# Kernel optimization log

Measured on AMD Instinct MI355X. Metric: run time of the kernel, lower is better.

Reference implementation:

```python
import jax, jax.numpy as jnp
import numpy as np

DIM = 1024
INTER = 1408
N_EXPERTS = 16
TOPK = 2
N_SHARED = 2
SHARED_INTER = N_SHARED * INTER
ROUTE_SCALE = 1.0


def setup_inputs() -> dict:
    key = jax.random.key(0)
    ks = jax.random.split(key, 16)
    s = 0.02
    return {
        "x": jax.random.normal(ks[0], (2, 2048, DIM), dtype=jnp.float32),
        "gate_w": jax.random.normal(ks[1], (DIM, N_EXPERTS), dtype=jnp.float32) * s,
        "gate_b": jnp.zeros((N_EXPERTS,), dtype=jnp.float32),
        "w1": jax.random.normal(ks[2], (N_EXPERTS, DIM, INTER), dtype=jnp.float32) * s,
        "b1": jnp.zeros((N_EXPERTS, INTER), dtype=jnp.float32),
        "w3": jax.random.normal(ks[3], (N_EXPERTS, DIM, INTER), dtype=jnp.float32) * s,
        "b3": jnp.zeros((N_EXPERTS, INTER), dtype=jnp.float32),
        "w2": jax.random.normal(ks[4], (N_EXPERTS, INTER, DIM), dtype=jnp.float32) * s,
        "b2": jnp.zeros((N_EXPERTS, DIM), dtype=jnp.float32),
        "sw1": jax.random.normal(ks[5], (DIM, SHARED_INTER), dtype=jnp.float32) * s,
        "sb1": jax.random.normal(ks[6], (SHARED_INTER,), dtype=jnp.float32) * s,
        "sw3": jax.random.normal(ks[7], (DIM, SHARED_INTER), dtype=jnp.float32) * s,
        "sb3": jax.random.normal(ks[8], (SHARED_INTER,), dtype=jnp.float32) * s,
        "sw2": jax.random.normal(ks[9], (SHARED_INTER, DIM), dtype=jnp.float32) * s,
        "sb2": jax.random.normal(ks[10], (DIM,), dtype=jnp.float32) * s,
    }


def reference(x, gate_w, gate_b, w1, b1, w3, b3, w2, b2, sw1, sb1, sw3, sb3, sw2, sb2):
    shape = x.shape
    xf = x.reshape(-1, DIM)  # [T, D]

    # Gate: softmax scores in fp32, top-k routing
    logits = xf @ gate_w + gate_b  # [T, E]
    scores = jax.nn.softmax(logits.astype(jnp.float32), axis=-1)
    top_vals, top_idx = jax.lax.top_k(scores, TOPK)  # [T, K]
    weights = (top_vals * ROUTE_SCALE).astype(x.dtype)

    # Combine weights per expert: [T, E]; zero for unselected experts
    cw = (jax.nn.one_hot(top_idx, N_EXPERTS, dtype=x.dtype) * weights[..., None]).sum(axis=1)

    # Routed experts (dense-per-expert SwiGLU, masked by combine weights)
    h = jnp.einsum('td,edh->teh', xf, w1) + b1  # [T, E, I]
    g = jnp.einsum('td,edh->teh', xf, w3) + b3
    a = jax.nn.silu(h) * g
    y = jnp.einsum('teh,ehd,te->td', a, w2, cw) + cw @ b2  # [T, D]

    # Shared expert SwiGLU
    z = (jax.nn.silu(xf @ sw1 + sb1) * (xf @ sw3 + sb3)) @ sw2 + sb2

    return (y + z).reshape(shape)
```

## Files before the change

### kernel.cpp

```cpp
#include <hip/hip_runtime.h>
#include <cstdint>
#include <cstddef>

#define T_TOKENS 4096
#define DIM      1024
#define INTER    1408
#define NEXP     16
#define SINTER   2816

typedef uint32_t u32;
typedef uint16_t u16;

using s8v = __attribute__((ext_vector_type(8))) short;
using f4v = __attribute__((ext_vector_type(4))) float;

__device__ __forceinline__ u16 f2bf(float f) {
  u32 u = __float_as_uint(f);
  return (u16)((u + 0x7fffu + ((u >> 16) & 1u)) >> 16);
}
__device__ __forceinline__ u32 pack2(float a, float b) {
  return (u32)f2bf(a) | ((u32)f2bf(b) << 16);
}

__device__ __forceinline__ void load_lds16(const u16* g, u16* l) {
  __builtin_amdgcn_global_load_lds((const __attribute__((address_space(1))) void*)g,
                                   (__attribute__((address_space(3))) void*)l,
                                   16, 0, 0);
}

__global__ __launch_bounds__(256)
void cvt_x(const float* __restrict__ in, u16* __restrict__ out) {
  const int i = (blockIdx.x * 256 + threadIdx.x) * 8;
  float4 a = *(const float4*)(in + i);
  float4 b = *(const float4*)(in + i + 4);
  uint4 o;
  o.x = pack2(a.x, a.y); o.y = pack2(a.z, a.w);
  o.z = pack2(b.x, b.y); o.w = pack2(b.z, b.w);
  *(uint4*)(out + i) = o;
}

__global__ __launch_bounds__(256)
void transpose_cvt(const float* __restrict__ in, u16* __restrict__ out,
                   int K, int N) {
  const size_t eoff = (size_t)blockIdx.z * K * N;
  const int n0 = blockIdx.x * 64, k0 = blockIdx.y * 64;
  __shared__ u16 t[64][72];

  const int tid = threadIdx.x;
  {
    const int r = tid >> 4, c4 = (tid & 15) * 4;
    const float* src = in + eoff + (size_t)k0 * N + n0;
#pragma unroll
    for (int i = 0; i < 4; i++) {
      int row = r + i * 16;
      float4 v = *(const float4*)(src + (size_t)row * N + c4);
      t[c4 + 0][row] = f2bf(v.x);
      t[c4 + 1][row] = f2bf(v.y);
      t[c4 + 2][row] = f2bf(v.z);
      t[c4 + 3][row] = f2bf(v.w);
    }
  }
  __syncthreads();
  {
    const int r = tid >> 3, cc = (tid & 7) * 8;
    u16* dst = out + eoff + (size_t)n0 * K + k0;
#pragma unroll
    for (int i = 0; i < 2; i++) {
      int row = r + i * 32;
      uint4 v = *(const uint4*)&t[row][cc];
      *(uint4*)(dst + (size_t)row * K + cc) = v;
    }
  }
}

__global__ __launch_bounds__(256)
void gate_logits(const float* __restrict__ x, const float* __restrict__ gw,
                 const float* __restrict__ gb,
                 int* __restrict__ g_e, float* __restrict__ g_w)
{
  const int tok  = blockIdx.x * 4 + (threadIdx.x >> 6);
  const int lane = threadIdx.x & 63;
  const int e = lane & 15, s = lane >> 4;
  const float* xr = x + (size_t)tok * DIM;

  float acc = 0.f;
#pragma unroll 8
  for (int i = 0; i < DIM / 4; i++) {
    const int k = i * 4 + s;
    acc = fmaf(xr[k], gw[i * 64 + lane], acc);
  }
  acc += __shfl_xor(acc, 16, 64);
  acc += __shfl_xor(acc, 32, 64);
  const float logit = acc + gb[e];

  float mx = logit;
#pragma unroll
  for (int o = 1; o < 16; o <<= 1) mx = fmaxf(mx, __shfl_xor(mx, o, 64));
  float p = __expf(logit - mx);
  float sum = p;
#pragma unroll
  for (int o = 1; o < 16; o <<= 1) sum += __shfl_xor(sum, o, 64);
  p /= sum;

  float m0 = p; int i0 = e;
#pragma unroll
  for (int o = 1; o < 16; o <<= 1) {
    float om = __shfl_xor(m0, o, 64); int oi = __shfl_xor(i0, o, 64);
    if (om > m0 || (om == m0 && oi < i0)) { m0 = om; i0 = oi; }
  }
  float p1 = (e == i0) ? -1.f : p;
  float m1 = p1; int i1 = e;
#pragma unroll
  for (int o = 1; o < 16; o <<= 1) {
    float om = __shfl_xor(m1, o, 64); int oi = __shfl_xor(i1, o, 64);
    if (om > m1 || (om == m1 && oi < i1)) { m1 = om; i1 = oi; }
  }
  if (lane == 0) {
    g_e[tok * 2 + 0] = i0;  g_e[tok * 2 + 1] = i1;
    g_w[tok * 2 + 0] = m0;  g_w[tok * 2 + 1] = m1;
  }
}

__global__ __launch_bounds__(256)
void route_build(const int* __restrict__ g_e,
                 int* __restrict__ offsets,
                 int* __restrict__ tok_slot, int* __restrict__ slot_of)
{
  __shared__ int hist[256][NEXP + 1];
  __shared__ int base[NEXP + 1];
  const int tid = threadIdx.x;
  const int TPT = T_TOKENS / 256;
  const int t0 = tid * TPT;

#pragma unroll
  for (int e = 0; e < NEXP; e++) hist[tid][e] = 0;
  for (int t = t0; t < t0 + TPT; t++) {
    hist[tid][g_e[t * 2 + 0]]++;
    hist[tid][g_e[t * 2 + 1]]++;
  }
  __syncthreads();
  if (tid < NEXP) {
    int run = 0;
    for (int i = 0; i < 256; i++) { int v = hist[i][tid]; hist[i][tid] = run; run += v; }
    base[tid] = run;
  }
  __syncthreads();
  if (tid == 0) {
    int run = 0;
#pragma unroll
    for (int e = 0; e < NEXP; e++) { int c = base[e]; base[e] = run; offsets[e] = run; run += c; }
    base[NEXP] = run; offsets[NEXP] = run;
  }
  __syncthreads();
  for (int t = t0; t < t0 + TPT; t++) {
#pragma unroll
    for (int k = 0; k < 2; k++) {
      const int e = g_e[t * 2 + k];
      const int slot = base[e] + hist[tid][e]++;
      tok_slot[slot] = t;
      slot_of[t * 2 + k] = slot;
    }
  }
}

template<bool GATHER>
__global__ __launch_bounds__(256, 2)
void ffn_up2(const u16* __restrict__ xbf,
             const u16* __restrict__ w1t, const float* __restrict__ b1p,
             const u16* __restrict__ w3t, const float* __restrict__ b3p,
             int N,
             const int* __restrict__ offsets, const int* __restrict__ tok_slot,
             u16* __restrict__ act)
{
  int e = 0, n0, mt;
  {
    const int lin = blockIdx.x;
    const int per = gridDim.x >> 3;
    const int xcd = lin & 7, pos = lin >> 3;
    if constexpr (GATHER) {
      const int half = per >> 1;
      const int sub = (pos >= half) ? 1 : 0;
      e = xcd * 2 + sub;
      const int idx = pos - sub * half;
      n0 = (idx >> 5) * 128;
      mt = idx & 31;
    } else {
      const int g = xcd * per + pos;
      n0 = (g >> 5) * 128;
      mt = g & 31;
    }
  }
  int rowbase = 0, count = T_TOKENS;
  if constexpr (GATHER) { rowbase = offsets[e]; count = offsets[e + 1] - rowbase; }
  const int m0 = mt * 128;
  if (m0 >= count) return;

  const u16* W1 = w1t + (size_t)e * N * DIM;
  const u16* W3 = w3t + (size_t)e * N * DIM;
  const float* B1 = b1p + (size_t)e * N;
  const float* B3 = b3p + (size_t)e * N;

  __shared__ u16 sA[2][128 * 32];
  __shared__ u16 sB1[2][128 * 32];
  __shared__ u16 sB3[2][128 * 32];

  const int tid = threadIdx.x;
  const int lane = tid & 63;
  const int w = tid >> 6;

  const int kc8 = (lane & 3) * 8;
  const u16* aptr[2]; const u16* b1ptr[2]; const u16* b3ptr[2];
  int ldoff[2];
#pragma unroll
  for (int i = 0; i < 2; i++) {
    const int row = i * 64 + w * 16 + (lane >> 2);
    ldoff[i] = i * 2048 + w * 512 + lane * 8;
    int arow = m0 + row; if (arow > count - 1) arow = count - 1;
    const int tok = GATHER ? tok_slot[rowbase + arow] : arow;
    aptr[i]  = xbf + (size_t)tok * DIM + kc8;
    const int brow = n0 + row;
    b1ptr[i] = W1 + (size_t)brow * DIM + kc8;
    b3ptr[i] = W3 + (size_t)brow * DIM + kc8;
  }

  const int ln = lane & 15, q = lane >> 4;
  const int wm = (w & 1) * 64, wn = (w >> 1) * 64;
  const int paOff = (wm + ln) * 32 + q * 8;
  const int pbOff = (wn + ln) * 32 + q * 8;

  f4v acc1[4][4] = {};
  f4v acc3[4][4] = {};

  auto stage = [&](int buf, int k0) {
#pragma unroll
    for (int i = 0; i < 2; i++) {
      load_lds16(aptr[i]  + k0, &sA[buf][ldoff[i]]);
      load_lds16(b1ptr[i] + k0, &sB1[buf][ldoff[i]]);
      load_lds16(b3ptr[i] + k0, &sB3[buf][ldoff[i]]);
    }
  };

  stage(0, 0);
  __syncthreads();
  int cur = 0;
  for (int k0 = 32; k0 <= DIM; k0 += 32) {
    if (k0 < DIM) stage(cur ^ 1, k0);

    const u16* pa  = sA[cur]  + paOff;
    const u16* pb1 = sB1[cur] + pbOff;
    const u16* pb3 = sB3[cur] + pbOff;
    s8v af[4];
#pragma unroll
    for (int i = 0; i < 4; i++) af[i] = *(const s8v*)(pa + i * 512);
#pragma unroll
    for (int j = 0; j < 4; j++) {
      s8v bf1 = *(const s8v*)(pb1 + j * 512);
#pragma unroll
      for (int i = 0; i < 4; i++)
        acc1[i][j] = __builtin_amdgcn_mfma_f32_16x16x32_bf16(af[i], bf1, acc1[i][j], 0, 0, 0);
      s8v bf3 = *(const s8v*)(pb3 + j * 512);
#pragma unroll
      for (int i = 0; i < 4; i++)
        acc3[i][j] = __builtin_amdgcn_mfma_f32_16x16x32_bf16(af[i], bf3, acc3[i][j], 0, 0, 0);
    }
    __syncthreads();
    cur ^= 1;
  }

  float bb1[4], bb3[4];
#pragma unroll
  for (int j = 0; j < 4; j++) {
    const int col = n0 + wn + j * 16 + ln;
    bb1[j] = B1[col]; bb3[j] = B3[col];
  }
#pragma unroll
  for (int i = 0; i < 4; i++) {
#pragma unroll
    for (int r = 0; r < 4; r++) {
      const int row = m0 + wm + i * 16 + q * 4 + r;
      if (row >= count) continue;
      u16* ap = act + (size_t)(rowbase + row) * N + n0 + wn;
#pragma unroll
      for (int j = 0; j < 4; j++) {
        float h = acc1[i][j][r] + bb1[j];
        float g = acc3[i][j][r] + bb3[j];
        float sv = 1.f / (1.f + __expf(-h));
        ap[j * 16 + ln] = f2bf(h * sv * g);
      }
    }
  }
}

template<bool ROUTED>
__global__ __launch_bounds__(256, 2)
void ffn_down2(const u16* __restrict__ act, int KA,
               const u16* __restrict__ w2t, const float* __restrict__ b2p,
               const int* __restrict__ offsets,
               float* __restrict__ outp)
{
  int e = 0, n0, mt;
  {
    const int lin = blockIdx.x;
    const int per = gridDim.x >> 3;
    const int xcd = lin & 7, pos = lin >> 3;
    if constexpr (ROUTED) {
      const int half = per >> 1;
      const int sub = (pos >= half) ? 1 : 0;
      e = xcd * 2 + sub;
      const int idx = pos - sub * half;
      n0 = (idx >> 5) * 128;
      mt = idx & 31;
    } else {
      const int g = xcd * per + pos;
      n0 = (g >> 5) * 128;
      mt = g & 31;
    }
  }
  int rowbase = 0, count = T_TOKENS;
  if constexpr (ROUTED) { rowbase = offsets[e]; count = offsets[e + 1] - rowbase; }
  const int m0 = mt * 128;
  if (m0 >= count) return;

  const u16* W2 = w2t + (size_t)e * DIM * KA;
  const float* B2 = b2p + (size_t)e * DIM;

  __shared__ u16 sA[2][128 * 32];
  __shared__ u16 sB[2][128 * 32];

  const int tid = threadIdx.x;
  const int lane = tid & 63;
  const int w = tid >> 6;

  const int kc8 = (lane & 3) * 8;
  const u16* aptr[2]; const u16* bptr[2];
  int ldoff[2];
#pragma unroll
  for (int i = 0; i < 2; i++) {
    const int row = i * 64 + w * 16 + (lane >> 2);
    ldoff[i] = i * 2048 + w * 512 + lane * 8;
    int arow = m0 + row; if (arow > count - 1) arow = count - 1;
    aptr[i] = act + (size_t)(rowbase + arow) * KA + kc8;
    bptr[i] = W2 + (size_t)(n0 + row) * KA + kc8;
  }

  const int ln = lane & 15, q = lane >> 4;
  const int wm = (w & 1) * 64, wn = (w >> 1) * 64;
  const int paOff = (wm + ln) * 32 + q * 8;
  const int pbOff = (wn + ln) * 32 + q * 8;

  f4v acc[4][4] = {};

  auto stage = [&](int buf, int k0) {
#pragma unroll
    for (int i = 0; i < 2; i++) {
      load_lds16(aptr[i] + k0, &sA[buf][ldoff[i]]);
      load_lds16(bptr[i] + k0, &sB[buf][ldoff[i]]);
    }
  };

  stage(0, 0);
  __syncthreads();
  int cur = 0;
  for (int k0 = 32; k0 <= KA; k0 += 32) {
    if (k0 < KA) stage(cur ^ 1, k0);

    const u16* pa = sA[cur] + paOff;
    const u16* pb = sB[cur] + pbOff;
    s8v af[4];
#pragma unroll
    for (int i = 0; i < 4; i++) af[i] = *(const s8v*)(pa + i * 512);
#pragma unroll
    for (int j = 0; j < 4; j++) {
      s8v bf = *(const s8v*)(pb + j * 512);
#pragma unroll
      for (int i = 0; i < 4; i++)
        acc[i][j] = __builtin_amdgcn_mfma_f32_16x16x32_bf16(af[i], bf, acc[i][j], 0, 0, 0);
    }
    __syncthreads();
    cur ^= 1;
  }

  float bb[4];
#pragma unroll
  for (int j = 0; j < 4; j++) bb[j] = B2[n0 + wn + j * 16 + ln];

#pragma unroll
  for (int i = 0; i < 4; i++) {
#pragma unroll
    for (int r = 0; r < 4; r++) {
      const int row = m0 + wm + i * 16 + q * 4 + r;
      if (row >= count) continue;
      float* orow = outp + (size_t)(rowbase + row) * DIM + n0 + wn;
#pragma unroll
      for (int j = 0; j < 4; j++)
        orow[j * 16 + ln] = acc[i][j][r] + bb[j];
    }
  }
}

__global__ __launch_bounds__(256)
void combine(const float* __restrict__ R, const int* __restrict__ slot_of,
             const float* __restrict__ g_w, float* __restrict__ out)
{
  const int t = blockIdx.x;
  const int c = threadIdx.x * 4;
  const int s0 = slot_of[t * 2 + 0], s1 = slot_of[t * 2 + 1];
  const float w0 = g_w[t * 2 + 0],  w1 = g_w[t * 2 + 1];
  float4 a = *(const float4*)(R + (size_t)s0 * DIM + c);
  float4 b = *(const float4*)(R + (size_t)s1 * DIM + c);
  float* op = out + (size_t)t * DIM + c;
  float4 o = *(const float4*)op;
  o.x += w0 * a.x + w1 * b.x;
  o.y += w0 * a.y + w1 * b.y;
  o.z += w0 * a.z + w1 * b.z;
  o.w += w0 * a.w + w1 * b.w;
  *(float4*)op = o;
}

extern "C" void kernel_launch(void* const* d_in, const int* in_sizes, int n_in,
                              void* d_out, int out_size, void* d_ws, size_t ws_size,
                              hipStream_t stream)
{
  const float* x   = (const float*)d_in[0];
  const float* gw  = (const float*)d_in[1];
  const float* gb  = (const float*)d_in[2];
  const float* w1  = (const float*)d_in[3];
  const float* b1  = (const float*)d_in[4];
  const float* w3  = (const float*)d_in[5];
  const float* b3  = (const float*)d_in[6];
  const float* w2  = (const float*)d_in[7];
  const float* b2  = (const float*)d_in[8];
  const float* sw1 = (const float*)d_in[9];
  const float* sb1 = (const float*)d_in[10];
  const float* sw3 = (const float*)d_in[11];
  const float* sb3 = (const float*)d_in[12];
  const float* sw2 = (const float*)d_in[13];
  const float* sb2 = (const float*)d_in[14];
  float* out = (float*)d_out;

  char* ws = (char*)d_ws;
  size_t off = 0;
  auto alloc = [&](size_t bytes) -> char* {
    off = (off + 255) & ~(size_t)255;
    char* p = ws + off;
    off += bytes;
    return p;
  };
  int*   offsets  = (int*)  alloc((NEXP + 1) * 4);
  int*   g_e      = (int*)  alloc((size_t)T_TOKENS * 2 * 4);
  float* g_w      = (float*)alloc((size_t)T_TOKENS * 2 * 4);
  int*   tok_slot = (int*)  alloc((size_t)T_TOKENS * 2 * 4);
  int*   slot_of  = (int*)  alloc((size_t)T_TOKENS * 2 * 4);
  u16*   xbf      = (u16*)  alloc((size_t)T_TOKENS * DIM * 2);
  u16*   w1t      = (u16*)  alloc((size_t)NEXP * INTER * DIM * 2);
  u16*   w3t      = (u16*)  alloc((size_t)NEXP * INTER * DIM * 2);
  u16*   w2t      = (u16*)  alloc((size_t)NEXP * DIM * INTER * 2);
  u16*   sw1t     = (u16*)  alloc((size_t)SINTER * DIM * 2);
  u16*   sw3t     = (u16*)  alloc((size_t)SINTER * DIM * 2);
  u16*   sw2t     = (u16*)  alloc((size_t)DIM * SINTER * 2);
  u16*   A_act    = (u16*)  alloc((size_t)T_TOKENS * 2 * INTER * 2);
  u16*   S_act    = (u16*)  alloc((size_t)T_TOKENS * SINTER * 2);
  float* Rbuf     = (float*)w1t;
  (void)ws_size; (void)in_sizes; (void)n_in; (void)out_size;

  gate_logits<<<T_TOKENS / 4, 256, 0, stream>>>(x, gw, gb, g_e, g_w);
  route_build<<<1, 256, 0, stream>>>(g_e, offsets, tok_slot, slot_of);

  cvt_x<<<(T_TOKENS * DIM) / (256 * 8), 256, 0, stream>>>(x, xbf);
  transpose_cvt<<<dim3(INTER / 64, DIM / 64, NEXP), 256, 0, stream>>>(w1, w1t, DIM, INTER);
  transpose_cvt<<<dim3(INTER / 64, DIM / 64, NEXP), 256, 0, stream>>>(w3, w3t, DIM, INTER);
  transpose_cvt<<<dim3(DIM / 64, INTER / 64, NEXP), 256, 0, stream>>>(w2, w2t, INTER, DIM);
  transpose_cvt<<<dim3(SINTER / 64, DIM / 64, 1), 256, 0, stream>>>(sw1, sw1t, DIM, SINTER);
  transpose_cvt<<<dim3(SINTER / 64, DIM / 64, 1), 256, 0, stream>>>(sw3, sw3t, DIM, SINTER);
  transpose_cvt<<<dim3(DIM / 64, SINTER / 64, 1), 256, 0, stream>>>(sw2, sw2t, SINTER, DIM);

  ffn_up2<false><<<(SINTER / 128) * 32, 256, 0, stream>>>(
      xbf, sw1t, sb1, sw3t, sb3, SINTER, nullptr, nullptr, S_act);
  ffn_down2<false><<<(DIM / 128) * 32, 256, 0, stream>>>(
      S_act, SINTER, sw2t, sb2, nullptr, out);

  ffn_up2<true><<<(INTER / 128) * 32 * NEXP, 256, 0, stream>>>(
      xbf, w1t, b1, w3t, b3, INTER, offsets, tok_slot, A_act);
  ffn_down2<true><<<(DIM / 128) * 32 * NEXP, 256, 0, stream>>>(
      A_act, INTER, w2t, b2, offsets, Rbuf);
  combine<<<T_TOKENS, 256, 0, stream>>>(Rbuf, slot_of, g_w, out);
}
```

Baseline: 699.2 us.

## Read A operand from global directly, double K-tile, swizzle B LDS, 3D grid

After: 1.484 ms. +112.2%, slower.

```diff
diff --git a/kernel.cpp b/kernel.cpp
--- a/kernel.cpp
+++ b/kernel.cpp
@@ -165,103 +165,91 @@
 
 template<bool GATHER>
 __global__ __launch_bounds__(256, 2)
-void ffn_up2(const u16* __restrict__ xbf,
+void ffn_up3(const u16* __restrict__ xbf,
              const u16* __restrict__ w1t, const float* __restrict__ b1p,
              const u16* __restrict__ w3t, const float* __restrict__ b3p,
              int N,
              const int* __restrict__ offsets, const int* __restrict__ tok_slot,
              u16* __restrict__ act)
 {
-  int e = 0, n0, mt;
-  {
-    const int lin = blockIdx.x;
-    const int per = gridDim.x >> 3;
-    const int xcd = lin & 7, pos = lin >> 3;
-    if constexpr (GATHER) {
-      const int half = per >> 1;
-      const int sub = (pos >= half) ? 1 : 0;
-      e = xcd * 2 + sub;
-      const int idx = pos - sub * half;
-      n0 = (idx >> 5) * 128;
-      mt = idx & 31;
-    } else {
-      const int g = xcd * per + pos;
-      n0 = (g >> 5) * 128;
-      mt = g & 31;
-    }
-  }
+  const int e = GATHER ? blockIdx.z : 0;
   int rowbase = 0, count = T_TOKENS;
   if constexpr (GATHER) { rowbase = offsets[e]; count = offsets[e + 1] - rowbase; }
-  const int m0 = mt * 128;
+  const int m0 = blockIdx.x * 128;
   if (m0 >= count) return;
+  const int n0 = blockIdx.y * 128;
 
   const u16* W1 = w1t + (size_t)e * N * DIM;
   const u16* W3 = w3t + (size_t)e * N * DIM;
   const float* B1 = b1p + (size_t)e * N;
   const float* B3 = b3p + (size_t)e * N;
 
-  __shared__ u16 sA[2][128 * 32];
-  __shared__ u16 sB1[2][128 * 32];
-  __shared__ u16 sB3[2][128 * 32];
-
-  const int tid = threadIdx.x;
-  const int lane = tid & 63;
-  const int w = tid >> 6;
-
-  const int kc8 = (lane & 3) * 8;
-  const u16* aptr[2]; const u16* b1ptr[2]; const u16* b3ptr[2];
-  int ldoff[2];
-#pragma unroll
-  for (int i = 0; i < 2; i++) {
-    const int row = i * 64 + w * 16 + (lane >> 2);
-    ldoff[i] = i * 2048 + w * 512 + lane * 8;
-    int arow = m0 + row; if (arow > count - 1) arow = count - 1;
-    const int tok = GATHER ? tok_slot[rowbase + arow] : arow;
-    aptr[i]  = xbf + (size_t)tok * DIM + kc8;
-    const int brow = n0 + row;
-    b1ptr[i] = W1 + (size_t)brow * DIM + kc8;
-    b3ptr[i] = W3 + (size_t)brow * DIM + kc8;
-  }
-
+  __shared__ u16 sB1[2][128 * 64];
+  __shared__ u16 sB3[2][128 * 64];
+
+  const int tid = threadIdx.x, lane = tid & 63, w = tid >> 6;
   const int ln = lane & 15, q = lane >> 4;
   const int wm = (w & 1) * 64, wn = (w >> 1) * 64;
-  const int paOff = (wm + ln) * 32 + q * 8;
-  const int pbOff = (wn + ln) * 32 + q * 8;
+
+  const int srow = w * 8 + (lane >> 3);
+  const int scol = ((lane & 7) ^ (lane >> 3)) * 8;
+  const u16* b1ptr[4]; const u16* b3ptr[4]; int ldoffB[4];
+#pragma unroll
+  for (int i = 0; i < 4; i++) {
+    const int row = i * 32 + srow;
+    ldoffB[i] = row * 64 + (lane & 7) * 8;
+    b1ptr[i] = W1 + (size_t)(n0 + row) * DIM + scol;
+    b3ptr[i] = W3 + (size_t)(n0 + row) * DIM + scol;
+  }
+
+  const u16* pA[4];
+#pragma unroll
+  for (int i = 0; i < 4; i++) {
+    int arow = m0 + wm + i * 16 + ln; if (arow > count - 1) arow = count - 1;
+    const int tok = GATHER ? tok_slot[rowbase + arow] : arow;
+    pA[i] = xbf + (size_t)tok * DIM + q * 8;
+  }
+
+  const int pbBase = (wn + ln) * 64;
+  const int swz0 = (q * 8) ^ ((ln & 7) * 8);
+  const int swz1 = (q * 8 + 32) ^ ((ln & 7) * 8);
 
   f4v acc1[4][4] = {};
   f4v acc3[4][4] = {};
 
   auto stage = [&](int buf, int k0) {
 #pragma unroll
-    for (int i = 0; i < 2; i++) {
-      load_lds16(aptr[i]  + k0, &sA[buf][ldoff[i]]);
-      load_lds16(b1ptr[i] + k0, &sB1[buf][ldoff[i]]);
-      load_lds16(b3ptr[i] + k0, &sB3[buf][ldoff[i]]);
+    for (int i = 0; i < 4; i++) {
+      load_lds16(b1ptr[i] + k0, &sB1[buf][ldoffB[i]]);
+      load_lds16(b3ptr[i] + k0, &sB3[buf][ldoffB[i]]);
     }
   };
 
   stage(0, 0);
   __syncthreads();
   int cur = 0;
-  for (int k0 = 32; k0 <= DIM; k0 += 32) {
+  for (int k0 = 64; k0 <= DIM; k0 += 64) {
     if (k0 < DIM) stage(cur ^ 1, k0);
-
-    const u16* pa  = sA[cur]  + paOff;
-    const u16* pb1 = sB1[cur] + pbOff;
-    const u16* pb3 = sB3[cur] + pbOff;
-    s8v af[4];
-#pragma unroll
-    for (int i = 0; i < 4; i++) af[i] = *(const s8v*)(pa + i * 512);
-#pragma unroll
-    for (int j = 0; j < 4; j++) {
-      s8v bf1 = *(const s8v*)(pb1 + j * 512);
-#pragma unroll
-      for (int i = 0; i < 4; i++)
-        acc1[i][j] = __builtin_amdgcn_mfma_f32_16x16x32_bf16(af[i], bf1, acc1[i][j], 0, 0, 0);
-      s8v bf3 = *(const s8v*)(pb3 + j * 512);
-#pragma unroll
-      for (int i = 0; i < 4; i++)
-        acc3[i][j] = __builtin_amdgcn_mfma_f32_16x16x32_bf16(af[i], bf3, acc3[i][j], 0, 0, 0);
+    const int kb = k0 - 64;
+#pragma unroll
+    for (int kk = 0; kk < 2; kk++) {
+      const int sw = kk ? swz1 : swz0;
+      s8v af[4];
+#pragma unroll
+      for (int i = 0; i < 4; i++) af[i] = *(const s8v*)(pA[i] + kb + kk * 32);
+      const u16* pb1 = &sB1[cur][pbBase + sw];
+      const u16* pb3 = &sB3[cur][pbBase + sw];
+#pragma unroll
+      for (int j = 0; j < 4; j++) {
+        s8v bf1 = *(const s8v*)(pb1 + j * 1024);
+#pragma unroll
+        for (int i = 0; i < 4; i++)
+          acc1[i][j] = __builtin_amdgcn_mfma_f32_16x16x32_bf16(af[i], bf1, acc1[i][j], 0, 0, 0);
+        s8v bf3 = *(const s8v*)(pb3 + j * 1024);
+#pragma unroll
+        for (int i = 0; i < 4; i++)
+          acc3[i][j] = __builtin_amdgcn_mfma_f32_16x16x32_bf16(af[i], bf3, acc3[i][j], 0, 0, 0);
+      }
     }
     __syncthreads();
     cur ^= 1;
@@ -292,89 +280,77 @@
 }
 
 template<bool ROUTED>
-__global__ __launch_bounds__(256, 2)
-void ffn_down2(const u16* __restrict__ act, int KA,
+__global__ __launch_bounds__(256, 3)
+void ffn_down3(const u16* __restrict__ act, int KA,
                const u16* __restrict__ w2t, const float* __restrict__ b2p,
                const int* __restrict__ offsets,
                float* __restrict__ outp)
 {
-  int e = 0, n0, mt;
-  {
-    const int lin = blockIdx.x;
-    const int per = gridDim.x >> 3;
-    const int xcd = lin & 7, pos = lin >> 3;
-    if constexpr (ROUTED) {
-      const int half = per >> 1;
-      const int sub = (pos >= half) ? 1 : 0;
-      e = xcd * 2 + sub;
-      const int idx = pos - sub * half;
-      n0 = (idx >> 5) * 128;
-      mt = idx & 31;
-    } else {
-      const int g = xcd * per + pos;
-      n0 = (g >> 5) * 128;
-      mt = g & 31;
-    }
-  }
+  const int e = ROUTED ? blockIdx.z : 0;
   int rowbase = 0, count = T_TOKENS;
   if constexpr (ROUTED) { rowbase = offsets[e]; count = offsets[e + 1] - rowbase; }
-  const int m0 = mt * 128;
+  const int m0 = blockIdx.x * 128;
   if (m0 >= count) return;
+  const int n0 = blockIdx.y * 128;
 
   const u16* W2 = w2t + (size_t)e * DIM * KA;
   const float* B2 = b2p + (size_t)e * DIM;
 
-  __shared__ u16 sA[2][128 * 32];
-  __shared__ u16 sB[2][128 * 32];
-
-  const int tid = threadIdx.x;
-  const int lane = tid & 63;
-  const int w = tid >> 6;
-
-  const int kc8 = (lane & 3) * 8;
-  const u16* aptr[2]; const u16* bptr[2];
-  int ldoff[2];
-#pragma unroll
-  for (int i = 0; i < 2; i++) {
-    const int row = i * 64 + w * 16 + (lane >> 2);
-    ldoff[i] = i * 2048 + w * 512 + lane * 8;
-    int arow = m0 + row; if (arow > count - 1) arow = count - 1;
-    aptr[i] = act + (size_t)(rowbase + arow) * KA + kc8;
-    bptr[i] = W2 + (size_t)(n0 + row) * KA + kc8;
-  }
-
+  __shared__ u16 sB[2][128 * 64];
+
+  const int tid = threadIdx.x, lane = tid & 63, w = tid >> 6;
   const int ln = lane & 15, q = lane >> 4;
   const int wm = (w & 1) * 64, wn = (w >> 1) * 64;
-  const int paOff = (wm + ln) * 32 + q * 8;
-  const int pbOff = (wn + ln) * 32 + q * 8;
+
+  const int srow = w * 8 + (lane >> 3);
+  const int scol = ((lane & 7) ^ (lane >> 3)) * 8;
+  const u16* bptr[4]; int ldoffB[4];
+#pragma unroll
+  for (int i = 0; i < 4; i++) {
+    const int row = i * 32 + srow;
+    ldoffB[i] = row * 64 + (lane & 7) * 8;
+    bptr[i] = W2 + (size_t)(n0 + row) * KA + scol;
+  }
+
+  const u16* pA[4];
+#pragma unroll
+  for (int i = 0; i < 4; i++) {
+    int arow = m0 + wm + i * 16 + ln; if (arow > count - 1) arow = count - 1;
+    pA[i] = act + (size_t)(rowbase + arow) * KA + q * 8;
+  }
+
+  const int pbBase = (wn + ln) * 64;
+  const int swz0 = (q * 8) ^ ((ln & 7) * 8);
+  const int swz1 = (q * 8 + 32) ^ ((ln & 7) * 8);
 
   f4v acc[4][4] = {};
 
   auto stage = [&](int buf, int k0) {
 #pragma unroll
-    for (int i = 0; i < 2; i++) {
-      load_lds16(aptr[i] + k0, &sA[buf][ldoff[i]]);
-      load_lds16(bptr[i] + k0, &sB[buf][ldoff[i]]);
-    }
+    for (int i = 0; i < 4; i++)
+      load_lds16(bptr[i] + k0, &sB[buf][ldoffB[i]]);
   };
 
   stage(0, 0);
   __syncthreads();
   int cur = 0;
-  for (int k0 = 32; k0 <= KA; k0 += 32) {
+  for (int k0 = 64; k0 <= KA; k0 += 64) {
     if (k0 < KA) stage(cur ^ 1, k0);
-
-    const u16* pa = sA[cur] + paOff;
-    const u16* pb = sB[cur] + pbOff;
-    s8v af[4];
-#pragma unroll
-    for (int i = 0; i < 4; i++) af[i] = *(const s8v*)(pa + i * 512);
-#pragma unroll
-    for (int j = 0; j < 4; j++) {
-      s8v bf = *(const s8v*)(pb + j * 512);
-#pragma unroll
-      for (int i = 0; i < 4; i++)
-        acc[i][j] = __builtin_amdgcn_mfma_f32_16x16x32_bf16(af[i], bf, acc[i][j], 0, 0, 0);
+    const int kb = k0 - 64;
+#pragma unroll
+    for (int kk = 0; kk < 2; kk++) {
+      const int sw = kk ? swz1 : swz0;
+      s8v af[4];
+#pragma unroll
+      for (int i = 0; i < 4; i++) af[i] = *(const s8v*)(pA[i] + kb + kk * 32);
+      const u16* pb = &sB[cur][pbBase + sw];
+#pragma unroll
+      for (int j = 0; j < 4; j++) {
+        s8v bf = *(const s8v*)(pb + j * 1024);
+#pragma unroll
+        for (int i = 0; i < 4; i++)
+          acc[i][j] = __builtin_amdgcn_mfma_f32_16x16x32_bf16(af[i], bf, acc[i][j], 0, 0, 0);
+      }
     }
     __syncthreads();
     cur ^= 1;
@@ -474,14 +450,14 @@
   transpose_cvt<<<dim3(SINTER / 64, DIM / 64, 1), 256, 0, stream>>>(sw3, sw3t, DIM, SINTER);
   transpose_cvt<<<dim3(DIM / 64, SINTER / 64, 1), 256, 0, stream>>>(sw2, sw2t, SINTER, DIM);
 
-  ffn_up2<false><<<(SINTER / 128) * 32, 256, 0, stream>>>(
+  ffn_up3<false><<<dim3(T_TOKENS / 128, SINTER / 128, 1), 256, 0, stream>>>(
       xbf, sw1t, sb1, sw3t, sb3, SINTER, nullptr, nullptr, S_act);
-  ffn_down2<false><<<(DIM / 128) * 32, 256, 0, stream>>>(
+  ffn_down3<false><<<dim3(T_TOKENS / 128, DIM / 128, 1), 256, 0, stream>>>(
       S_act, SINTER, sw2t, sb2, nullptr, out);
 
-  ffn_up2<true><<<(INTER / 128) * 32 * NEXP, 256, 0, stream>>>(
+  ffn_up3<true><<<dim3(T_TOKENS / 128, INTER / 128, NEXP), 256, 0, stream>>>(
       xbf, w1t, b1, w3t, b3, INTER, offsets, tok_slot, A_act);
-  ffn_down2<true><<<(DIM / 128) * 32 * NEXP, 256, 0, stream>>>(
+  ffn_down3<true><<<dim3(T_TOKENS / 128, DIM / 128, NEXP), 256, 0, stream>>>(
       A_act, INTER, w2t, b2, offsets, Rbuf);
   combine<<<T_TOKENS, 256, 0, stream>>>(Rbuf, slot_of, g_w, out);
 }
```
